# Kernel tuning notes

Hardware: AMD Instinct MI355X
Metric: run time of the kernel (lower is better)

## Reference

```python
import jax, jax.numpy as jnp
import numpy as np

NUM_CLASSES = 100
FEATURE_DIM = 128
N_SAMPLES = 1_000_000
EPS = 1e-8  # matches F.cosine_similarity eps clamp


def setup_inputs() -> dict:
    key = jax.random.key(0)
    k1, k2 = jax.random.split(key)
    train_feature = jax.random.normal(k1, (N_SAMPLES, FEATURE_DIM), dtype=jnp.float32)
    train_label = jax.random.randint(k2, (N_SAMPLES,), 0, NUM_CLASSES, dtype=jnp.int64)
    return {"train_feature": train_feature, "train_label": train_label}


def reference(train_feature, train_label):
    # Original math per class c with n = |c| samples:
    #   A[i,j] = cos(f_i, f_j) for i != j, then A /= (n-1) (if n > 1)
    #   P_c = (sum_k mean(A[k]) * f_k) / n
    # Key identity: row_sum_k of the cosine matrix (excluding diagonal)
    #   = u_k . (sum_{j in c} u_j) - u_k . u_k, where u = f / max(||f||, eps).
    # So no N x N matrix is ever needed -- pure segment reductions.
    labels = train_label.astype(jnp.int32)
    norms = jnp.linalg.norm(train_feature, axis=1, keepdims=True)
    u = train_feature / jnp.maximum(norms, EPS)  # [N, d] unit vectors

    counts = jax.ops.segment_sum(
        jnp.ones((train_feature.shape[0],), dtype=train_feature.dtype),
        labels, num_segments=NUM_CLASSES)  # [C]
    m = jax.ops.segment_sum(u, labels, num_segments=NUM_CLASSES)  # [C, d]

    n_c = counts[labels]  # [N] class size per sample
    self_sim = jnp.sum(u * u, axis=1)  # == 1 for nonzero rows (0 if f == 0)
    row_sum = jnp.sum(u * m[labels], axis=1) - self_sim  # [N]

    # weight_k = row_mean(A)_k = row_sum / ((n-1) * n); n==1 gives row_sum == 0
    denom = jnp.maximum(n_c - 1.0, 1.0) * jnp.maximum(n_c, 1.0)
    w = row_sum / denom  # [N]

    proto_sum = jax.ops.segment_sum(w[:, None] * train_feature, labels,
                                    num_segments=NUM_CLASSES)  # [C, d]
    prototypes = proto_sum / jnp.maximum(counts, 1.0)[:, None]
    return prototypes
```

## Files before the change

### kernel.cpp

```cpp
#include <hip/hip_runtime.h>


namespace {

constexpr int C = 100;
constexpr int D = 128;
constexpr float EPS = 1e-8f;
constexpr int BLOCK = 256;
constexpr int GRID = 768;
constexpr int S = 8;

__global__ __launch_bounds__(BLOCK) void k_stats(const float4* __restrict__ feat4,
                                                 const int* __restrict__ lab,
                                                 float* __restrict__ m_g,
                                                 float* __restrict__ cnt_g,
                                                 int n) {
  __shared__ float m_loc[C * D];
  __shared__ float cnt_loc[C];
  for (int i = threadIdx.x; i < C * D; i += BLOCK) m_loc[i] = 0.f;
  if (threadIdx.x < C) cnt_loc[threadIdx.x] = 0.f;
  __syncthreads();

  const int lane = threadIdx.x & 63;
  const int half = lane >> 5;
  const int sl = lane & 31;
  const int wid = (blockIdx.x * BLOCK + threadIdx.x) >> 6;
  const int nw = (GRID * BLOCK) >> 6;

  for (int base = wid * S; base < n; base += nw * S) {
    float4 x[4];
    int c[4];
    bool valid[4];
#pragma unroll
    for (int s = 0; s < 4; ++s) {
      int idx = base + 2 * s + half;
      valid[s] = idx < n;
      int ci = valid[s] ? idx : n - 1;
      x[s] = feat4[(size_t)ci * 32 + sl];
      c[s] = lab[ci];
    }
    float ss[4];
#pragma unroll
    for (int s = 0; s < 4; ++s)
      ss[s] = x[s].x * x[s].x + x[s].y * x[s].y + x[s].z * x[s].z + x[s].w * x[s].w;
#pragma unroll
    for (int off = 16; off > 0; off >>= 1) {
#pragma unroll
      for (int s = 0; s < 4; ++s) ss[s] += __shfl_xor(ss[s], off, 64);
    }
#pragma unroll
    for (int s = 0; s < 4; ++s) {
      if (!valid[s]) continue;
      float inv = 1.0f / fmaxf(sqrtf(ss[s]), EPS);
      float* mp = &m_loc[c[s] * D];
      atomicAdd(&mp[0 * 32 + sl], x[s].x * inv);
      atomicAdd(&mp[1 * 32 + sl], x[s].y * inv);
      atomicAdd(&mp[2 * 32 + sl], x[s].z * inv);
      atomicAdd(&mp[3 * 32 + sl], x[s].w * inv);
      if (sl == 0) atomicAdd(&cnt_loc[c[s]], 1.0f);
    }
  }
  __syncthreads();

  for (int i = threadIdx.x; i < C * D; i += BLOCK) {
    int cls = i >> 7, a = i & 127, q = a >> 5, s2 = a & 31;
    atomicAdd(&m_g[cls * D + s2 * 4 + q], m_loc[i]);
  }
  if (threadIdx.x < C) atomicAdd(&cnt_g[threadIdx.x], cnt_loc[threadIdx.x]);
}

__global__ __launch_bounds__(BLOCK) void k_proto(const float4* __restrict__ feat4,
                                                 const int* __restrict__ lab,
                                                 const float4* __restrict__ m_g4,
                                                 const float* __restrict__ cnt_g,
                                                 float* __restrict__ proto_g,
                                                 int n) {
  __shared__ float p_loc[C * D];
  __shared__ float cnt_loc[C];
  for (int i = threadIdx.x; i < C * D; i += BLOCK) p_loc[i] = 0.f;
  if (threadIdx.x < C) cnt_loc[threadIdx.x] = cnt_g[threadIdx.x];
  __syncthreads();

  const int lane = threadIdx.x & 63;
  const int half = lane >> 5;
  const int sl = lane & 31;
  const int wid = (blockIdx.x * BLOCK + threadIdx.x) >> 6;
  const int nw = (GRID * BLOCK) >> 6;

  for (int base = wid * S; base < n; base += nw * S) {
    float4 x[4], mv[4];
    int c[4];
    bool valid[4];
#pragma unroll
    for (int s = 0; s < 4; ++s) {
      int idx = base + 2 * s + half;
      valid[s] = idx < n;
      int ci = valid[s] ? idx : n - 1;
      x[s] = feat4[(size_t)ci * 32 + sl];
      c[s] = lab[ci];
    }
#pragma unroll
    for (int s = 0; s < 4; ++s) mv[s] = m_g4[c[s] * 32 + sl];

    float ss[4], pm[4];
#pragma unroll
    for (int s = 0; s < 4; ++s) {
      ss[s] = x[s].x * x[s].x + x[s].y * x[s].y + x[s].z * x[s].z + x[s].w * x[s].w;
      pm[s] = x[s].x * mv[s].x + x[s].y * mv[s].y + x[s].z * mv[s].z + x[s].w * mv[s].w;
    }
#pragma unroll
    for (int off = 16; off > 0; off >>= 1) {
#pragma unroll
      for (int s = 0; s < 4; ++s) {
        ss[s] += __shfl_xor(ss[s], off, 64);
        pm[s] += __shfl_xor(pm[s], off, 64);
      }
    }
#pragma unroll
    for (int s = 0; s < 4; ++s) {
      if (!valid[s]) continue;
      float inv = 1.0f / fmaxf(sqrtf(ss[s]), EPS);
      float row_sum = pm[s] * inv - ss[s] * inv * inv;
      float nc = cnt_loc[c[s]];
      float w = row_sum / (fmaxf(nc - 1.f, 1.f) * fmaxf(nc, 1.f));
      float* pp = &p_loc[c[s] * D];
      atomicAdd(&pp[0 * 32 + sl], w * x[s].x);
      atomicAdd(&pp[1 * 32 + sl], w * x[s].y);
      atomicAdd(&pp[2 * 32 + sl], w * x[s].z);
      atomicAdd(&pp[3 * 32 + sl], w * x[s].w);
    }
  }
  __syncthreads();

  for (int i = threadIdx.x; i < C * D; i += BLOCK) {
    int cls = i >> 7, a = i & 127, q = a >> 5, s2 = a & 31;
    atomicAdd(&proto_g[cls * D + s2 * 4 + q], p_loc[i]);
  }
}

__global__ void k_final(const float* __restrict__ proto_g,
                        const float* __restrict__ cnt_g,
                        float* __restrict__ out) {
  int i = blockIdx.x * BLOCK + threadIdx.x;
  if (i < C * D) out[i] = proto_g[i] / fmaxf(cnt_g[i / D], 1.f);
}

}

extern "C" void kernel_launch(void* const* d_in, const int* in_sizes, int n_in,
                              void* d_out, int out_size, void* d_ws, size_t ws_size,
                              hipStream_t stream) {
  const float* feat = (const float*)d_in[0];
  const int* lab = (const int*)d_in[1];
  const int n = in_sizes[0] / D;

  float* m_g = (float*)d_ws;
  float* cnt_g = m_g + C * D;
  float* proto_g = cnt_g + C;
  hipMemsetAsync(d_ws, 0, (size_t)(2 * C * D + C) * sizeof(float), stream);

  k_stats<<<GRID, BLOCK, 0, stream>>>((const float4*)feat, lab, m_g, cnt_g, n);
  k_proto<<<GRID, BLOCK, 0, stream>>>((const float4*)feat, lab, (const float4*)m_g,
                                      cnt_g, proto_g, n);
  k_final<<<(C * D + BLOCK - 1) / BLOCK, BLOCK, 0, stream>>>(proto_g, cnt_g, (float*)d_out);
}
```

Baseline: 1.914 ms.

## Replace global atomic merges with per-block partial slots and split reduction kernels

Each block now writes its shared-memory class sums to a private workspace slot instead of doing atomics on the global accumulators. A separate split reduction kernel then sums the slots, and the final division by class count is folded into the per-sample weight, which removes the final kernel. The block size is doubled to 512. This is meant to cut global atomic contention from 768 blocks all hitting the same 12.8K addresses, at the cost of extra workspace traffic and two more launches. If the workspace is too small, the code falls back to atomics.

```diff
diff --git a/kernel.cpp b/kernel.cpp
--- a/kernel.cpp
+++ b/kernel.cpp
@@ -6,15 +6,17 @@
 constexpr int C = 100;
 constexpr int D = 128;
 constexpr float EPS = 1e-8f;
-constexpr int BLOCK = 256;
+constexpr int BLOCK = 512;
 constexpr int GRID = 768;
 constexpr int S = 8;
+constexpr int SLOT_F = C * D + 128;
+constexpr int RED_SPLIT = 8;
 
 __global__ __launch_bounds__(BLOCK) void k_stats(const float4* __restrict__ feat4,
                                                  const int* __restrict__ lab,
-                                                 float* __restrict__ m_g,
-                                                 float* __restrict__ cnt_g,
-                                                 int n) {
+                                                 float* __restrict__ partial,
+                                                 float* __restrict__ mcnt_g,
+                                                 int n, int mode) {
   __shared__ float m_loc[C * D];
   __shared__ float cnt_loc[C];
   for (int i = threadIdx.x; i < C * D; i += BLOCK) m_loc[i] = 0.f;
@@ -62,19 +64,30 @@
   }
   __syncthreads();
 
-  for (int i = threadIdx.x; i < C * D; i += BLOCK) {
-    int cls = i >> 7, a = i & 127, q = a >> 5, s2 = a & 31;
-    atomicAdd(&m_g[cls * D + s2 * 4 + q], m_loc[i]);
-  }
-  if (threadIdx.x < C) atomicAdd(&cnt_g[threadIdx.x], cnt_loc[threadIdx.x]);
+  if (mode) {
+    float* slot = partial + (size_t)blockIdx.x * SLOT_F;
+    for (int i = threadIdx.x; i < C * D; i += BLOCK) {
+      int cls = i >> 7, a = i & 127, q = a >> 5, s2 = a & 31;
+      slot[cls * D + s2 * 4 + q] = m_loc[i];
+    }
+    for (int i = threadIdx.x; i < SLOT_F - C * D; i += BLOCK)
+      slot[C * D + i] = (i < C) ? cnt_loc[i] : 0.f;
+  } else {
+    for (int i = threadIdx.x; i < C * D; i += BLOCK) {
+      int cls = i >> 7, a = i & 127, q = a >> 5, s2 = a & 31;
+      atomicAdd(&mcnt_g[cls * D + s2 * 4 + q], m_loc[i]);
+    }
+    if (threadIdx.x < C) atomicAdd(&mcnt_g[C * D + threadIdx.x], cnt_loc[threadIdx.x]);
+  }
 }
 
 __global__ __launch_bounds__(BLOCK) void k_proto(const float4* __restrict__ feat4,
                                                  const int* __restrict__ lab,
                                                  const float4* __restrict__ m_g4,
                                                  const float* __restrict__ cnt_g,
-                                                 float* __restrict__ proto_g,
-                                                 int n) {
+                                                 float* __restrict__ partial,
+                                                 float* __restrict__ out,
+                                                 int n, int mode) {
   __shared__ float p_loc[C * D];
   __shared__ float cnt_loc[C];
   for (int i = threadIdx.x; i < C * D; i += BLOCK) p_loc[i] = 0.f;
@@ -122,7 +135,7 @@
       float inv = 1.0f / fmaxf(sqrtf(ss[s]), EPS);
       float row_sum = pm[s] * inv - ss[s] * inv * inv;
       float nc = cnt_loc[c[s]];
-      float w = row_sum / (fmaxf(nc - 1.f, 1.f) * fmaxf(nc, 1.f));
+      float w = row_sum / (fmaxf(nc - 1.f, 1.f) * fmaxf(nc, 1.f) * fmaxf(nc, 1.f));
       float* pp = &p_loc[c[s] * D];
       atomicAdd(&pp[0 * 32 + sl], w * x[s].x);
       atomicAdd(&pp[1 * 32 + sl], w * x[s].y);
@@ -132,17 +145,32 @@
   }
   __syncthreads();
 
-  for (int i = threadIdx.x; i < C * D; i += BLOCK) {
-    int cls = i >> 7, a = i & 127, q = a >> 5, s2 = a & 31;
-    atomicAdd(&proto_g[cls * D + s2 * 4 + q], p_loc[i]);
-  }
-}
-
-__global__ void k_final(const float* __restrict__ proto_g,
-                        const float* __restrict__ cnt_g,
-                        float* __restrict__ out) {
-  int i = blockIdx.x * BLOCK + threadIdx.x;
-  if (i < C * D) out[i] = proto_g[i] / fmaxf(cnt_g[i / D], 1.f);
+  if (mode) {
+    float* slot = partial + (size_t)blockIdx.x * SLOT_F;
+    for (int i = threadIdx.x; i < C * D; i += BLOCK) {
+      int cls = i >> 7, a = i & 127, q = a >> 5, s2 = a & 31;
+      slot[cls * D + s2 * 4 + q] = p_loc[i];
+    }
+  } else {
+    for (int i = threadIdx.x; i < C * D; i += BLOCK) {
+      int cls = i >> 7, a = i & 127, q = a >> 5, s2 = a & 31;
+      atomicAdd(&out[cls * D + s2 * 4 + q], p_loc[i]);
+    }
+  }
+}
+
+__global__ void k_reduce(const float* __restrict__ partial, float* __restrict__ dst,
+                         int width, int stride, int nslots) {
+  int i = blockIdx.x * blockDim.x + threadIdx.x;
+  if (i >= width) return;
+  int chunk = (nslots + gridDim.y - 1) / gridDim.y;
+  int p0 = blockIdx.y * chunk;
+  int p1 = p0 + chunk;
+  if (p1 > nslots) p1 = nslots;
+  float acc = 0.f;
+#pragma unroll 8
+  for (int p = p0; p < p1; ++p) acc += partial[(size_t)p * stride + i];
+  atomicAdd(&dst[i], acc);
 }
 
 }
@@ -154,13 +182,22 @@
   const int* lab = (const int*)d_in[1];
   const int n = in_sizes[0] / D;
 
-  float* m_g = (float*)d_ws;
-  float* cnt_g = m_g + C * D;
-  float* proto_g = cnt_g + C;
-  hipMemsetAsync(d_ws, 0, (size_t)(2 * C * D + C) * sizeof(float), stream);
-
-  k_stats<<<GRID, BLOCK, 0, stream>>>((const float4*)feat, lab, m_g, cnt_g, n);
-  k_proto<<<GRID, BLOCK, 0, stream>>>((const float4*)feat, lab, (const float4*)m_g,
-                                      cnt_g, proto_g, n);
-  k_final<<<(C * D + BLOCK - 1) / BLOCK, BLOCK, 0, stream>>>(proto_g, cnt_g, (float*)d_out);
-}
+  float* mcnt = (float*)d_ws;
+  float* partial = mcnt + SLOT_F;
+  const size_t need = (size_t)(GRID + 1) * SLOT_F * sizeof(float);
+  const int mode = (ws_size >= need) ? 1 : 0;
+
+  hipMemsetAsync(mcnt, 0, SLOT_F * sizeof(float), stream);
+  hipMemsetAsync(d_out, 0, out_size, stream);
+
+  k_stats<<<GRID, BLOCK, 0, stream>>>((const float4*)feat, lab, partial, mcnt, n, mode);
+  if (mode)
+    k_reduce<<<dim3((SLOT_F + 255) / 256, RED_SPLIT), 256, 0, stream>>>(
+        partial, mcnt, SLOT_F, SLOT_F, GRID);
+
+  k_proto<<<GRID, BLOCK, 0, stream>>>((const float4*)feat, lab, (const float4*)mcnt,
+                                      mcnt + C * D, partial, (float*)d_out, n, mode);
+  if (mode)
+    k_reduce<<<dim3((C * D + 255) / 256, RED_SPLIT), 256, 0, stream>>>(
+        partial, (float*)d_out, C * D, SLOT_F, GRID);
+}
```

Result: no change. 1.906 ms (-0.5%).
